# Optimization experiments

Measured on AMD Instinct MI355X. Metric: run time of the kernel, lower is better.

Reference implementation:

```python
import jax, jax.numpy as jnp
import numpy as np
from functools import partial
from jax import lax

STRIDE = 32
INPUT_SIZE = 448
SIZE = INPUT_SIZE // STRIDE  # 14
RATIOS = [[4, 4], [3, 5], [5, 3], [6, 6], [5, 7], [7, 5], [8, 8], [6, 10], [10, 6], [7, 9], [9, 7], [7, 10], [10, 7]]
N_LIST = [2, 3, 2]
IOU_THRESHS = [0.25, 0.25, 0.25]
PROPOSAL_N = sum(N_LIST)  # 7


def _make_coords():
    # Reproduces indices2coordinates/ComputeCoordinate exactly (incl. the
    # lefttop clamp happening AFTER rightlow is computed).
    coords = []
    for (rh, rw) in RATIOS:
        hw = SIZE - rh + 1
        ww = SIZE - rw + 1
        idx = np.arange(hw * ww)
        xi = idx // ww
        yi = idx % ww
        x1 = xi * STRIDE - 1
        y1 = yi * STRIDE - 1
        x2 = x1 + rh * STRIDE
        y2 = y1 + rw * STRIDE
        x1 = np.maximum(x1, 0)
        y1 = np.maximum(y1, 0)
        coords.append(np.stack([x1, y1, x2, y2], axis=1))
    return np.concatenate(coords, axis=0).astype(np.float32)

COORDS = jnp.asarray(_make_coords())  # [917, 4]
WINDOW_NUMS = [(SIZE - rh + 1) * (SIZE - rw + 1) for (rh, rw) in RATIOS]
GROUP_BOUNDS = [0, sum(WINDOW_NUMS[:3]), sum(WINDOW_NUMS[:6]), sum(WINDOW_NUMS)]  # [0,361,602,917]


def _all_window_scores(x):
    # sum over channels commutes with spatial avgpool -> pool the channel-sum.
    s = x.sum(axis=1)  # [B, 14, 14]
    parts = []
    for (rh, rw) in RATIOS:
        p = lax.reduce_window(s, 0.0, lax.add, (1, rh, rw), (1, 1, 1), 'VALID') / float(rh * rw)
        parts.append(p.reshape(s.shape[0], -1))
    return jnp.concatenate(parts, axis=1)  # [B, 917]


def _group_nms(scores, coords, n_sel, thresh):
    # Greedy NMS: iteratively pick argmax, suppress IoU > thresh. scores: [W].
    areas = (coords[:, 2] - coords[:, 0] + 1.0) * (coords[:, 3] - coords[:, 1] + 1.0)
    ar = jnp.arange(scores.shape[0])

    def step(sc, _):
        i = jnp.argmax(sc)
        b = coords[i]
        x1 = jnp.maximum(coords[:, 0], b[0])
        y1 = jnp.maximum(coords[:, 1], b[1])
        x2 = jnp.minimum(coords[:, 2], b[2])
        y2 = jnp.minimum(coords[:, 3], b[3])
        lw = x2 - x1 + 1.0
        lh = y2 - y1 + 1.0
        inter = jnp.where((lw < 0) | (lh < 0), 0.0, lw * lh)
        iou = inter / (areas + areas[i] - inter)
        sc_new = jnp.where((iou > thresh) | (ar == i), -jnp.inf, sc)
        return sc_new, i

    _, idxs = lax.scan(step, scores, None, length=n_sel)
    return idxs  # [n_sel] int


def setup_inputs() -> dict:
    key = jax.random.key(0)
    x = jax.random.normal(key, (64, 2048, SIZE, SIZE), dtype=jnp.float32)
    return {"x": x}


def reference(x):
    all_scores = _all_window_scores(x)            # [B, 917]
    det = lax.stop_gradient(all_scores)
    idx_groups = []
    for j in range(3):
        lo, hi = GROUP_BOUNDS[j], GROUP_BOUNDS[j + 1]
        f = partial(_group_nms, coords=COORDS[lo:hi], n_sel=N_LIST[j], thresh=IOU_THRESHS[j])
        idxs = jax.vmap(f)(det[:, lo:hi]) + lo     # [B, N_j]
        idx_groups.append(idxs)
    proposalN_indices = jnp.concatenate(idx_groups, axis=1)          # [B, 7]
    proposalN_windows_scores = jnp.take_along_axis(all_scores, proposalN_indices, axis=1)  # [B, 7]
    window_scores = all_scores                                        # [B, 917]
    return proposalN_indices, proposalN_windows_scores, window_scores
```

## Files before the change

kernel.cpp:

```cpp
#include <hip/hip_runtime.h>
#include <math.h>

#define NCH    2048
#define SZ     14
#define NPOS   (SZ*SZ)
#define NQ     (NPOS/4)
#define F4B    (NCH*NQ)
#define TACT   980
#define NITER  102
#define TAILN  392
#define NWIN   917
#define NB     64
#define PN     7
#define KPER   6

__global__ __launch_bounds__(1024) void k_appm(const float4* __restrict__ x,
                                               float* __restrict__ out) {
  const int b    = blockIdx.x;
  const int tid  = threadIdx.x;
  const int lane = tid & 63;
  const int wave = tid >> 6;

  __shared__ float4 red[20][NQ];
  __shared__ float  s[NPOS];
  __shared__ float  sc[NWIN];
  __shared__ float  bx1[NWIN], by1[NWIN], bx2[NWIN], by2[NWIN], bar[NWIN];

  const int rh[13] = {4,3,5,6,5,7,8,6,10,7,9,7,10};
  const int rw[13] = {4,5,3,6,7,5,8,10,6,9,7,10,7};
  const int wb[14] = {0,121,241,361,442,522,602,651,696,741,789,837,877,917};

  if (tid < TACT) {
    const size_t base = (size_t)b * F4B;
    float ax = 0.f, ay = 0.f, az = 0.f, aw = 0.f;
#pragma unroll 17
    for (int i = 0; i < NITER; ++i) {
      const float4 v = x[base + (size_t)i * TACT + tid];
      ax += v.x; ay += v.y; az += v.z; aw += v.w;
    }
    if (tid < TAILN) {
      const float4 v = x[base + 99960 + tid];
      ax += v.x; ay += v.y; az += v.z; aw += v.w;
    }
    float4 o; o.x = ax; o.y = ay; o.z = az; o.w = aw;
    red[tid / NQ][tid % NQ] = o;
  }
  __syncthreads();

  if (tid < NQ) {
    float ax = 0.f, ay = 0.f, az = 0.f, aw = 0.f;
#pragma unroll
    for (int r = 0; r < 20; ++r) {
      const float4 v = red[r][tid];
      ax += v.x; ay += v.y; az += v.z; aw += v.w;
    }
    s[tid * 4 + 0] = ax; s[tid * 4 + 1] = ay;
    s[tid * 4 + 2] = az; s[tid * 4 + 3] = aw;
  }
  __syncthreads();

  if (tid < NWIN) {
    const int w = tid;
    int r = 0;
    while (w >= wb[r + 1]) ++r;
    const int l  = w - wb[r];
    const int RH = rh[r], RW = rw[r];
    const int ww = SZ - RW + 1;
    const int xi = l / ww, yi = l % ww;
    float sum = 0.f;
    for (int i = 0; i < RH; ++i)
      for (int j = 0; j < RW; ++j)
        sum += s[(xi + i) * SZ + (yi + j)];
    const float score = sum / (float)(RH * RW);
    sc[w] = score;
    out[NB * PN * 2 + b * NWIN + w] = score;
    float x1 = (float)(xi * 32 - 1);
    float y1 = (float)(yi * 32 - 1);
    float x2 = x1 + (float)(RH * 32);
    float y2 = y1 + (float)(RW * 32);
    if (x1 < 0.f) x1 = 0.f;
    if (y1 < 0.f) y1 = 0.f;
    bx1[w] = x1; by1[w] = y1; bx2[w] = x2; by2[w] = y2;
    bar[w] = (x2 - x1 + 1.f) * (y2 - y1 + 1.f);
  }
  __syncthreads();

  if (wave < 3) {
    const int glo[3] = {0, 361, 602};
    const int ghi[3] = {361, 602, 917};
    const int gns[3] = {2, 3, 2};
    const int gob[3] = {0, 2, 5};
    const int lo = glo[wave], hi = ghi[wave];
    const int nsel = gns[wave], obase = gob[wave];

    float wk[KPER], X1[KPER], Y1[KPER], X2[KPER], Y2[KPER], AR[KPER];
#pragma unroll
    for (int k = 0; k < KPER; ++k) {
      const int j = lo + lane + k * 64;
      const bool v = j < hi;
      const int jj = v ? j : lo;
      wk[k] = v ? sc[jj] : -INFINITY;
      X1[k] = bx1[jj]; Y1[k] = by1[jj];
      X2[k] = bx2[jj]; Y2[k] = by2[jj]; AR[k] = bar[jj];
    }

    for (int st = 0; st < nsel; ++st) {
      float bv = -INFINITY; int bj = 0x7fffffff;
#pragma unroll
      for (int k = 0; k < KPER; ++k) {
        const int j = lo + lane + k * 64;
        if (wk[k] > bv) { bv = wk[k]; bj = j; }
      }
      for (int off = 32; off > 0; off >>= 1) {
        const float ov = __shfl_xor(bv, off);
        const int   oj = __shfl_xor(bj, off);
        if (ov > bv || (ov == bv && oj < bj)) { bv = ov; bj = oj; }
      }
      const float sx1 = bx1[bj], sy1 = by1[bj];
      const float sx2 = bx2[bj], sy2 = by2[bj], sar = bar[bj];
      if (lane == 0) {
        out[b * PN + obase + st]           = (float)bj;
        out[NB * PN + b * PN + obase + st] = sc[bj];
      }
#pragma unroll
      for (int k = 0; k < KPER; ++k) {
        const int j = lo + lane + k * 64;
        const float ix1 = fmaxf(X1[k], sx1);
        const float iy1 = fmaxf(Y1[k], sy1);
        const float ix2 = fminf(X2[k], sx2);
        const float iy2 = fminf(Y2[k], sy2);
        const float lw = ix2 - ix1 + 1.f;
        const float lh = iy2 - iy1 + 1.f;
        const float inter = (lw < 0.f || lh < 0.f) ? 0.f : lw * lh;
        const float iou = inter / (AR[k] + sar - inter);
        if (iou > 0.25f || j == bj) wk[k] = -INFINITY;
      }
    }
  }
}

extern "C" void kernel_launch(void* const* d_in, const int* in_sizes, int n_in,
                              void* d_out, int out_size, void* d_ws, size_t ws_size,
                              hipStream_t stream) {
  const float4* x = (const float4*)d_in[0];
  float* out = (float*)d_out;
  k_appm<<<NB, 1024, 0, stream>>>(x, out);
}
```

Measured before the change: 33.55 us.

## Split channel reduction across more blocks with separate NMS kernel

Splits the per-batch channel sum into four blocks per batch, each reducing 512 channels and writing partial spatial sums to workspace. A second kernel adds the four partials and then runs window scoring and NMS. The aim is to raise memory-level parallelism from 64 blocks to 256 blocks so more CUs stream the 51MB input. The cost is an extra kernel launch and a small workspace round-trip.

```diff
diff --git a/kernel.cpp b/kernel.cpp
--- a/kernel.cpp
+++ b/kernel.cpp
@@ -5,57 +5,76 @@
 #define SZ     14
 #define NPOS   (SZ*SZ)
 #define NQ     (NPOS/4)
-#define F4B    (NCH*NQ)
-#define TACT   980
-#define NITER  102
-#define TAILN  392
-#define NWIN   917
 #define NB     64
 #define PN     7
+#define NWIN   917
 #define KPER   6
 
-__global__ __launch_bounds__(1024) void k_appm(const float4* __restrict__ x,
-                                               float* __restrict__ out) {
+#define QPB    4
+#define CPB    512
+#define F4PB   (CPB*NQ)
+#define TACT   980
+#define NIT    25
+#define TAILN  588
+
+__global__ __launch_bounds__(1024) void k_chansum(const float4* __restrict__ x,
+                                                  float4* __restrict__ part4) {
+  const int b = blockIdx.x;
+  const int q = blockIdx.y;
+  const int t = threadIdx.x;
+
+  __shared__ float4 red[20][NQ];
+
+  if (t < TACT) {
+    const size_t base = (size_t)b * (NCH * NQ) + (size_t)q * F4PB;
+    float ax = 0.f, ay = 0.f, az = 0.f, aw = 0.f;
+#pragma unroll 5
+    for (int i = 0; i < NIT; ++i) {
+      const float4 v = x[base + (size_t)i * TACT + t];
+      ax += v.x; ay += v.y; az += v.z; aw += v.w;
+    }
+    if (t < TAILN) {
+      const float4 v = x[base + 24500 + t];
+      ax += v.x; ay += v.y; az += v.z; aw += v.w;
+    }
+    float4 o; o.x = ax; o.y = ay; o.z = az; o.w = aw;
+    red[t / NQ][t % NQ] = o;
+  }
+  __syncthreads();
+
+  if (t < NQ) {
+    float ax = 0.f, ay = 0.f, az = 0.f, aw = 0.f;
+#pragma unroll
+    for (int r = 0; r < 20; ++r) {
+      const float4 v = red[r][t];
+      ax += v.x; ay += v.y; az += v.z; aw += v.w;
+    }
+    float4 o; o.x = ax; o.y = ay; o.z = az; o.w = aw;
+    part4[(b * QPB + q) * NQ + t] = o;
+  }
+}
+
+__global__ __launch_bounds__(1024) void k_nms(const float* __restrict__ part,
+                                              float* __restrict__ out) {
   const int b    = blockIdx.x;
   const int tid  = threadIdx.x;
   const int lane = tid & 63;
   const int wave = tid >> 6;
 
-  __shared__ float4 red[20][NQ];
-  __shared__ float  s[NPOS];
-  __shared__ float  sc[NWIN];
-  __shared__ float  bx1[NWIN], by1[NWIN], bx2[NWIN], by2[NWIN], bar[NWIN];
+  __shared__ float s[NPOS];
+  __shared__ float sc[NWIN];
+  __shared__ float bx1[NWIN], by1[NWIN], bx2[NWIN], by2[NWIN], bar[NWIN];
 
   const int rh[13] = {4,3,5,6,5,7,8,6,10,7,9,7,10};
   const int rw[13] = {4,5,3,6,7,5,8,10,6,9,7,10,7};
   const int wb[14] = {0,121,241,361,442,522,602,651,696,741,789,837,877,917};
 
-  if (tid < TACT) {
-    const size_t base = (size_t)b * F4B;
-    float ax = 0.f, ay = 0.f, az = 0.f, aw = 0.f;
-#pragma unroll 17
-    for (int i = 0; i < NITER; ++i) {
-      const float4 v = x[base + (size_t)i * TACT + tid];
-      ax += v.x; ay += v.y; az += v.z; aw += v.w;
-    }
-    if (tid < TAILN) {
-      const float4 v = x[base + 99960 + tid];
-      ax += v.x; ay += v.y; az += v.z; aw += v.w;
-    }
-    float4 o; o.x = ax; o.y = ay; o.z = az; o.w = aw;
-    red[tid / NQ][tid % NQ] = o;
-  }
-  __syncthreads();
-
-  if (tid < NQ) {
-    float ax = 0.f, ay = 0.f, az = 0.f, aw = 0.f;
+  if (tid < NPOS) {
+    const float* p = part + (size_t)b * QPB * NPOS + tid;
+    float acc = 0.f;
 #pragma unroll
-    for (int r = 0; r < 20; ++r) {
-      const float4 v = red[r][tid];
-      ax += v.x; ay += v.y; az += v.z; aw += v.w;
-    }
-    s[tid * 4 + 0] = ax; s[tid * 4 + 1] = ay;
-    s[tid * 4 + 2] = az; s[tid * 4 + 3] = aw;
+    for (int q = 0; q < QPB; ++q) acc += p[q * NPOS];
+    s[tid] = acc;
   }
   __syncthreads();
 
@@ -144,5 +163,9 @@
                               hipStream_t stream) {
   const float4* x = (const float4*)d_in[0];
   float* out = (float*)d_out;
-  k_appm<<<NB, 1024, 0, stream>>>(x, out);
+  float4* part4 = (float4*)d_ws;
+
+  dim3 g1(NB, QPB);
+  k_chansum<<<g1, 1024, 0, stream>>>(x, part4);
+  k_nms<<<NB, 1024, 0, stream>>>((const float*)d_ws, out);
 }
```

After: 30.85 us. -8.1%, faster.
